# Optimization experiments

Measured on AMD Instinct MI355X. Metric: run time of the kernel, lower is better.

Reference implementation:

```python
import jax, jax.numpy as jnp
import numpy as np

EPS = 1e-5

def layernorm(x, gamma, beta):
    mu = jnp.mean(x, axis=-1, keepdims=True)
    var = jnp.var(x, axis=-1, keepdims=True)
    return (x - mu) * jax.lax.rsqrt(var + EPS) * gamma + beta

def setup_inputs() -> dict:
    key = jax.random.key(0)
    ks = jax.random.split(key, 8)
    B, N, D, H, Dh, M = 2, 2048, 768, 12, 64, 3072
    s = 0.02
    return {
        "x": jax.random.normal(ks[0], (B, N, D), jnp.float32),
        "Wqkv": jax.random.normal(ks[1], (D, 3 * H * Dh), jnp.float32) * s,
        "Wout": jax.random.normal(ks[2], (H * Dh, D), jnp.float32) * s,
        "gamma1": jnp.ones((D,), jnp.float32),
        "beta1": jnp.zeros((D,), jnp.float32),
        "gamma2": jnp.ones((D,), jnp.float32),
        "beta2": jnp.zeros((D,), jnp.float32),
        "W1": jax.random.normal(ks[3], (D, M), jnp.float32) * s,
        "b1": jnp.zeros((M,), jnp.float32),
        "W2": jax.random.normal(ks[4], (M, D), jnp.float32) * s,
        "b2": jnp.zeros((D,), jnp.float32),
        "attn_bias": jax.random.normal(ks[5], (1, H, N, N), jnp.float32) * 0.1,
    }

def reference(x, Wqkv, Wout, gamma1, beta1, gamma2, beta2, W1, b1, W2, b2, attn_bias):
    B, N, D = x.shape
    H = attn_bias.shape[1]
    Dh = Wqkv.shape[1] // (3 * H)
    scale = Dh ** -0.5
    # Attention block (pre-norm)
    h = layernorm(x, gamma1, beta1)
    qkv = h @ Wqkv                              # [B, N, 3*H*Dh]
    qkv = qkv.reshape(B, N, 3, H, Dh)
    q, k, v = (jnp.transpose(qkv[:, :, i], (0, 2, 1, 3)) for i in range(3))  # [B, H, N, Dh]
    dots = jnp.einsum('bhqd,bhkd->bhqk', q, k) * scale
    # pos_info == 'mul_att_normed'
    attn = jax.nn.softmax(dots, axis=-1) * jax.nn.softmax(attn_bias, axis=-1)
    attn = attn / jnp.sum(attn, axis=-1, keepdims=True)
    out = jnp.einsum('bhqk,bhkd->bhqd', attn, v)          # [B, H, N, Dh]
    out = jnp.transpose(out, (0, 2, 1, 3)).reshape(B, N, H * Dh)
    x = out @ Wout + x
    # FeedForward block (pre-norm)
    h = layernorm(x, gamma2, beta2)
    h = jax.nn.gelu(h @ W1 + b1, approximate=False)
    x = h @ W2 + b2 + x
    return x
```

## Files before the change

### kernel.cpp

```cpp
#include <hip/hip_runtime.h>

typedef unsigned short u16t;
typedef __bf16 bf16x8 __attribute__((ext_vector_type(8)));
typedef float  f32x4  __attribute__((ext_vector_type(4)));
typedef float  f32x16 __attribute__((ext_vector_type(16)));
typedef unsigned u32x2 __attribute__((ext_vector_type(2)));
typedef unsigned u32x4 __attribute__((ext_vector_type(4)));

#define DEV __device__ __forceinline__

DEV u16t f32_to_bf16(float f) {
    unsigned u = __float_as_uint(f);
    unsigned r = (u + 0x7FFFu + ((u >> 16) & 1u)) >> 16;
    return (u16t)r;
}
DEV float bf16_to_f32(u16t u) { return __uint_as_float((unsigned)u << 16); }

DEV unsigned cvt_pk_bf16(float lo, float hi) {
    unsigned r;
    asm("v_cvt_pk_bf16_f32 %0, %1, %2" : "=v"(r) : "v"(lo), "v"(hi));
    return r;
}

DEV float gelu_exact(float x) {
    return 0.5f * x * (1.0f + erff(x * 0.70710678118654752f));
}

DEV void glds16(const void* g, void* l) {
    __builtin_amdgcn_global_load_lds(
        (const __attribute__((address_space(1))) void*)g,
        (__attribute__((address_space(3))) void*)l, 16, 0, 0);
}

#define SCHED_FENCE() __builtin_amdgcn_sched_barrier(0)

#define WAITN_BARRIER(N)                                          \
    asm volatile("s_waitcnt vmcnt(" #N ")" ::: "memory");         \
    SCHED_FENCE();                                                \
    __builtin_amdgcn_s_barrier();                                 \
    SCHED_FENCE();

#define PLAIN_BARRIER()                                           \
    SCHED_FENCE();                                                \
    __builtin_amdgcn_s_barrier();                                 \
    SCHED_FENCE();

__global__ __launch_bounds__(256)
void ln_kernel(const float* __restrict__ x, const float* __restrict__ g,
               const float* __restrict__ b, u16t* __restrict__ out)
{
    const int row = blockIdx.x;
    const int t = threadIdx.x;
    const float* xr = x + (size_t)row * 768;
    float v0 = xr[t], v1 = xr[t + 256], v2 = xr[t + 512];
    float s = v0 + v1 + v2;
    float s2 = v0 * v0 + v1 * v1 + v2 * v2;
#pragma unroll
    for (int off = 32; off > 0; off >>= 1) {
        s  += __shfl_xor(s, off);
        s2 += __shfl_xor(s2, off);
    }
    __shared__ float sm[8];
    const int w = t >> 6;
    if ((t & 63) == 0) { sm[w] = s; sm[4 + w] = s2; }
    __syncthreads();
    s  = sm[0] + sm[1] + sm[2] + sm[3];
    s2 = sm[4] + sm[5] + sm[6] + sm[7];
    const float mu  = s * (1.0f / 768.0f);
    const float var = fmaxf(s2 * (1.0f / 768.0f) - mu * mu, 0.0f);
    const float rst = rsqrtf(var + 1e-5f);
    u16t* o = out + (size_t)row * 768;
    o[t]       = f32_to_bf16((v0 - mu) * rst * g[t]       + b[t]);
    o[t + 256] = f32_to_bf16((v1 - mu) * rst * g[t + 256] + b[t + 256]);
    o[t + 512] = f32_to_bf16((v2 - mu) * rst * g[t + 512] + b[t + 512]);
}

__global__ __launch_bounds__(256)
void transpose_all(const float* __restrict__ Wqkv, const float* __restrict__ Wout,
                   const float* __restrict__ W1, const float* __restrict__ W2,
                   u16t* __restrict__ WqkvT, u16t* __restrict__ WoutT,
                   u16t* __restrict__ W1T, u16t* __restrict__ W2T)
{
    int b = blockIdx.x;
    const float* in; u16t* out; int R, C, cx, ry;
    if (b < 432)       { in = Wqkv; out = WqkvT; R = 768;  C = 2304; cx = b % 36; ry = b / 36; }
    else if (b < 576)  { b -= 432;  in = Wout; out = WoutT; R = 768;  C = 768;  cx = b % 12; ry = b / 12; }
    else if (b < 1152) { b -= 576;  in = W1;   out = W1T;   R = 768;  C = 3072; cx = b % 48; ry = b / 48; }
    else               { b -= 1152; in = W2;   out = W2T;   R = 3072; C = 768;  cx = b % 12; ry = b / 12; }
    __shared__ float tile[64][65];
    const int c0 = cx * 64, r0 = ry * 64;
    const int t = threadIdx.x;
#pragma unroll
    for (int j = 0; j < 16; ++j) {
        const int idx = j * 256 + t;
        const int rl = idx >> 6, cl = idx & 63;
        tile[rl][cl] = in[(size_t)(r0 + rl) * C + c0 + cl];
    }
    __syncthreads();
#pragma unroll
    for (int j = 0; j < 16; ++j) {
        const int idx = j * 256 + t;
        const int cl = idx >> 6, rl = idx & 63;
        out[(size_t)(c0 + cl) * R + r0 + rl] = f32_to_bf16(tile[rl][cl]);
    }
}

template <int MODE, int TM>
__global__ __launch_bounds__(256)
void gemm_kernel(const u16t* __restrict__ A, const u16t* __restrict__ BT,
                 float* __restrict__ Cf, u16t* __restrict__ Cb,
                 const float* __restrict__ bias, const float* __restrict__ res,
                 u16t* __restrict__ Qo, u16t* __restrict__ Ko,
                 u16t* __restrict__ VTo,
                 int M, int Nn, int K)
{
    constexpr int MI = TM / 32;
    constexpr int ABYTES = TM * 64;
    constexpr int BUFB = ABYTES + 8192;
    __shared__ __align__(16) char gsm[2 * BUFB];
    const int t = threadIdx.x;
    const int w = t >> 6, lane = t & 63;
    const int l16 = lane & 15, lhi = lane >> 4;
    const int wr = w >> 1, wc = w & 1;
    const int m0 = blockIdx.x * TM, n0 = blockIdx.y * 128;

    const f32x4 fz = {0.f, 0.f, 0.f, 0.f};
    f32x4 acc[MI][4];
#pragma unroll
    for (int i = 0; i < MI; ++i)
#pragma unroll
        for (int j = 0; j < 4; ++j) acc[i][j] = fz;

    const int srow = lane >> 2;
    const int sslot = ((lane & 3) ^ ((lane >> 3) & 3)) * 16;
    const int aswz = ((lhi ^ ((l16 >> 1) & 3)) << 4);

    auto stage = [&](int bufb, int kt) {
#pragma unroll
        for (int i = 0; i < TM / 64; ++i) {
            const int row = w * (TM / 4) + i * 16 + srow;
            glds16((const char*)A + ((size_t)(m0 + row) * K + kt) * 2 + sslot,
                   gsm + bufb + w * (TM * 16) + i * 1024);
        }
#pragma unroll
        for (int i = 0; i < 2; ++i) {
            const int row = w * 32 + i * 16 + srow;
            glds16((const char*)BT + ((size_t)(n0 + row) * K + kt) * 2 + sslot,
                   gsm + bufb + ABYTES + w * 2048 + i * 1024);
        }
    };

    auto body = [&](int bufb) {
        const char* Ab = gsm + bufb;
        const char* Bb = gsm + bufb + ABYTES;
        bf16x8 af[MI], bfv[4];
#pragma unroll
        for (int i = 0; i < MI; ++i)
            af[i] = *reinterpret_cast<const bf16x8*>(
                Ab + (16 * MI * wr + 16 * i + l16) * 64 + aswz);
#pragma unroll
        for (int j = 0; j < 4; ++j)
            bfv[j] = *reinterpret_cast<const bf16x8*>(
                Bb + (64 * wc + 16 * j + l16) * 64 + aswz);
#pragma unroll
        for (int i = 0; i < MI; ++i)
#pragma unroll
            for (int j = 0; j < 4; ++j)
                acc[i][j] = __builtin_amdgcn_mfma_f32_16x16x32_bf16(
                    af[i], bfv[j], acc[i][j], 0, 0, 0);
    };

    stage(0, 0);
    int bufb = 0;
    for (int kt = 0; kt + 32 < K; kt += 32) {
        stage(bufb ^ BUFB, kt + 32);
        if constexpr (TM == 128) { WAITN_BARRIER(4) }
        else                     { WAITN_BARRIER(3) }
        body(bufb);
        PLAIN_BARRIER()
        bufb ^= BUFB;
    }
    WAITN_BARRIER(0)
    body(bufb);

    const int rb = m0 + 16 * MI * wr + 4 * lhi;
    const int cb = n0 + 64 * wc + l16;

    if constexpr (MODE == 3) {
        const int qi = n0 / 768;
        const int b = rb >> 11;
        const int nn0 = rb & 2047;
#pragma unroll
        for (int j = 0; j < 4; ++j) {
            const int c = cb - qi * 768 + 16 * j;
            const int h = c >> 6, d = c & 63;
            if (qi < 2) {
                u16t* dst = (qi == 0) ? Qo : Ko;
                const size_t base = ((size_t)(b * 12 + h) * 2048 + nn0) * 64 + d;
#pragma unroll
                for (int i = 0; i < MI; ++i)
#pragma unroll
                    for (int r = 0; r < 4; ++r)
                        dst[base + (size_t)(16 * i + r) * 64] =
                            f32_to_bf16(acc[i][j][r]);
            } else {
                u16t* dst = VTo + ((size_t)(b * 12 + h) * 64 + d) * 2048 + nn0;
#pragma unroll
                for (int i = 0; i < MI; ++i) {
                    u32x2 pr;
                    pr[0] = cvt_pk_bf16(acc[i][j][0], acc[i][j][1]);
                    pr[1] = cvt_pk_bf16(acc[i][j][2], acc[i][j][3]);
                    *reinterpret_cast<u32x2*>(dst + 16 * i) = pr;
                }
            }
        }
        return;
    }

#pragma unroll
    for (int i = 0; i < MI; ++i) {
#pragma unroll
        for (int j = 0; j < 4; ++j) {
#pragma unroll
            for (int r = 0; r < 4; ++r) {
                const int row = rb + 16 * i + r;
                const int col = cb + 16 * j;
                float v = acc[i][j][r];
                if (MODE == 0) {
                    Cf[(size_t)row * Nn + col] = v;
                } else if (MODE == 1) {
                    v += res[(size_t)row * Nn + col];
                    if (bias) v += bias[col];
                    Cf[(size_t)row * Nn + col] = v;
                } else if (MODE == 2) {
                    v = gelu_exact(v + bias[col]);
                    Cb[(size_t)row * Nn + col] = f32_to_bf16(v);
                }
            }
        }
    }
}

__global__ __launch_bounds__(256, 2)
void attn_kernel(const u16t* __restrict__ Q, const u16t* __restrict__ K,
                 const u16t* __restrict__ VT, const float* __restrict__ bias,
                 u16t* __restrict__ Opart, float* __restrict__ Lpart)
{
    const int SEQ = 2048;
    const int h = blockIdx.y;
    const int ks = blockIdx.z;
    const int t = threadIdx.x;
    const int w = t >> 6, lane = t & 63;
    const int l32 = lane & 31, hi = lane >> 5;
    const int q = blockIdx.x * 128 + w * 32 + l32;
    const int bh0 = h, bh1 = 12 + h;

    __shared__ __align__(16) char smem[65536];

    const u16t* qp0 = Q + ((size_t)bh0 * SEQ + q) * 64 + 8 * hi;
    const u16t* qp1 = Q + ((size_t)bh1 * SEQ + q) * 64 + 8 * hi;
    bf16x8 qf0[4], qf1[4];
#pragma unroll
    for (int dseg = 0; dseg < 4; ++dseg) {
        qf0[dseg] = *reinterpret_cast<const bf16x8*>(qp0 + dseg * 16);
        qf1[dseg] = *reinterpret_cast<const bf16x8*>(qp1 + dseg * 16);
    }

    const char* kg0 = (const char*)K + (size_t)bh0 * SEQ * 128;
    const char* kg1 = (const char*)K + (size_t)bh1 * SEQ * 128;
    const char* vg0 = (const char*)VT + (size_t)bh0 * 64 * 4096;
    const char* vg1 = (const char*)VT + (size_t)bh1 * 64 * 4096;
    const char* bg = (const char*)bias +
                     ((size_t)h * SEQ + blockIdx.x * 128) * 8192;

    const int srow8 = lane >> 3;
    const int sslotK = ((lane & 7) ^ srow8) * 16;
    const int vrow  = w * 16 + (lane >> 2);
    const int sslotV = ((lane & 3) ^ ((vrow >> 1) & 3)) * 16;

    auto stage_all = [&](int bb, int k0) {
#pragma unroll
        for (int i = 0; i < 4; ++i) {
            const int row = 32 * w + 8 * i + srow8;
            glds16(bg + (size_t)row * 8192 + (size_t)k0 * 4 + sslotK,
                   smem + bb + 4096 * w + i * 1024);
        }
        glds16(kg0 + (size_t)(k0 + 8 * w + srow8) * 128 + sslotK,
               smem + bb + 16384 + w * 1024);
        glds16(kg1 + (size_t)(k0 + 8 * w + srow8) * 128 + sslotK,
               smem + bb + 20480 + w * 1024);
        glds16(vg0 + (size_t)vrow * 4096 + (size_t)k0 * 2 + sslotV,
               smem + bb + 24576 + w * 1024);
        glds16(vg1 + (size_t)vrow * 4096 + (size_t)k0 * 2 + sslotV,
               smem + bb + 28672 + w * 1024);
    };

    const int rsw = l32 & 7;
    int boff[4], koff[4];
#pragma unroll
    for (int g = 0; g < 4; ++g)
        boff[g] = (32 * w + l32) * 128 + ((((g << 1) + hi) ^ rsw) << 4);
#pragma unroll
    for (int dseg = 0; dseg < 4; ++dseg)
        koff[dseg] = l32 * 128 + ((((dseg << 1) + hi) ^ rsw) << 4);
    const int vr3 = (l32 >> 1) & 3;
    const int voff00 = l32 * 64 + ((hi ^ vr3) << 4);
    const int voff01 = l32 * 64 + (((2 + hi) ^ vr3) << 4);
    const int voff10 = voff00 + 32 * 64;
    const int voff11 = voff01 + 32 * 64;

    f32x16 o00, o01, o10, o11;
#pragma unroll
    for (int i = 0; i < 16; ++i) { o00[i] = 0.f; o01[i] = 0.f;
                                   o10[i] = 0.f; o11[i] = 0.f; }
    float lsum0 = 0.f, lsum1 = 0.f;

    auto batch_body = [&](const bf16x8 (&qf)[4], int kvbase, int vbase,
                          const f32x4 (&bv)[4], f32x16& oa, f32x16& ob,
                          float& lsum) {
        f32x16 st;
#pragma unroll
        for (int i = 0; i < 16; ++i) st[i] = 0.f;
#pragma unroll
        for (int dseg = 0; dseg < 4; ++dseg) {
            bf16x8 kf = *reinterpret_cast<const bf16x8*>(
                smem + kvbase + koff[dseg]);
            st = __builtin_amdgcn_mfma_f32_32x32x16_bf16(kf, qf[dseg], st, 0, 0, 0);
        }
        unsigned pk[8];
#pragma unroll
        for (int i2 = 0; i2 < 8; ++i2) {
            const int ia = 2 * i2, ib = 2 * i2 + 1;
            const float pa = __expf(st[ia] * 0.125f + bv[ia >> 2][ia & 3]);
            const float pb = __expf(st[ib] * 0.125f + bv[ib >> 2][ib & 3]);
            lsum += pa + pb;
            pk[i2] = cvt_pk_bf16(pa, pb);
        }
        unsigned sx[8];
#pragma unroll
        for (int i2 = 0; i2 < 8; ++i2)
            sx[i2] = (unsigned)__shfl_xor((int)pk[i2], 32);
        union { unsigned u[4]; bf16x8 v; } B0, B1;
        B0.u[0] = hi ? sx[2] : pk[0];
        B0.u[1] = hi ? sx[3] : pk[1];
        B0.u[2] = hi ? pk[2] : sx[0];
        B0.u[3] = hi ? pk[3] : sx[1];
        B1.u[0] = hi ? sx[6] : pk[4];
        B1.u[1] = hi ? sx[7] : pk[5];
        B1.u[2] = hi ? pk[6] : sx[4];
        B1.u[3] = hi ? pk[7] : sx[5];
        bf16x8 v00 = *reinterpret_cast<const bf16x8*>(smem + vbase + voff00);
        bf16x8 v01 = *reinterpret_cast<const bf16x8*>(smem + vbase + voff01);
        bf16x8 v10 = *reinterpret_cast<const bf16x8*>(smem + vbase + voff10);
        bf16x8 v11 = *reinterpret_cast<const bf16x8*>(smem + vbase + voff11);
        oa = __builtin_amdgcn_mfma_f32_32x32x16_bf16(v00, B0.v, oa, 0, 0, 0);
        oa = __builtin_amdgcn_mfma_f32_32x32x16_bf16(v01, B1.v, oa, 0, 0, 0);
        ob = __builtin_amdgcn_mfma_f32_32x32x16_bf16(v10, B0.v, ob, 0, 0, 0);
        ob = __builtin_amdgcn_mfma_f32_32x32x16_bf16(v11, B1.v, ob, 0, 0, 0);
    };

    const int kbeg = ks * 512;

    stage_all(0, kbeg);
    WAITN_BARRIER(0)

    int cur = 0;
    for (int i = 0; i < 16; ++i) {
        const int k0 = kbeg + 32 * i;
        if (i < 15) {
            stage_all(cur ^ 32768, k0 + 32);
            WAITN_BARRIER(8)
        } else {
            WAITN_BARRIER(0)
        }
        {
            f32x4 bv[4];
#pragma unroll
            for (int g = 0; g < 4; ++g)
                bv[g] = *reinterpret_cast<const f32x4*>(smem + cur + boff[g]);
            batch_body(qf0, cur + 16384, cur + 24576, bv, o00, o01, lsum0);
            batch_body(qf1, cur + 20480, cur + 28672, bv, o10, o11, lsum1);
        }
        PLAIN_BARRIER()
        cur ^= 32768;
    }

    lsum0 += __shfl_xor(lsum0, 32);
    lsum1 += __shfl_xor(lsum1, 32);

#pragma unroll
    for (int beta = 0; beta < 2; ++beta) {
        const int bh = beta ? bh1 : bh0;
        const f32x16& oa = beta ? o10 : o00;
        const f32x16& ob = beta ? o11 : o01;
        const float ls = beta ? lsum1 : lsum0;
        u16t* op = Opart + ((size_t)(ks * 24 + bh) * SEQ + q) * 64;
#pragma unroll
        for (int dh = 0; dh < 2; ++dh) {
            const f32x16& o = dh ? ob : oa;
#pragma unroll
            for (int g = 0; g < 4; ++g) {
                u32x2 pr;
                pr[0] = cvt_pk_bf16(o[4 * g], o[4 * g + 1]);
                pr[1] = cvt_pk_bf16(o[4 * g + 2], o[4 * g + 3]);
                *reinterpret_cast<u32x2*>(op + dh * 32 + 8 * g + 4 * hi) = pr;
            }
        }
        if (!hi)
            Lpart[(size_t)(ks * 24 + bh) * SEQ + q] = ls;
    }
}

__global__ __launch_bounds__(256)
void attn_combine(const u16t* __restrict__ Opart,
                  const float* __restrict__ Lpart, u16t* __restrict__ out)
{
    const int idx = blockIdx.x * 256 + threadIdx.x;
    const int dg = idx & 7;
    const int q = (idx >> 3) & 2047;
    const int bh = idx >> 14;
    const int b = bh / 12, h = bh % 12;
    const size_t base = ((size_t)bh * 2048 + q) * 64 + dg * 8;
    const size_t stride = (size_t)24 * 2048 * 64;
    float acc[8] = {0.f, 0.f, 0.f, 0.f, 0.f, 0.f, 0.f, 0.f};
    float l = 0.f;
#pragma unroll
    for (int j = 0; j < 4; ++j) {
        const u32x4 a = *reinterpret_cast<const u32x4*>(Opart + base + j * stride);
#pragma unroll
        for (int m = 0; m < 4; ++m) {
            acc[2 * m]     += bf16_to_f32((u16t)(a[m] & 0xFFFF));
            acc[2 * m + 1] += bf16_to_f32((u16t)(a[m] >> 16));
        }
        l += Lpart[(size_t)j * 24 * 2048 + bh * 2048 + q];
    }
    const float inv = 1.0f / l;
    u32x4 r;
#pragma unroll
    for (int m = 0; m < 4; ++m)
        r[m] = cvt_pk_bf16(acc[2 * m] * inv, acc[2 * m + 1] * inv);
    *reinterpret_cast<u32x4*>(
        out + ((size_t)(b * 2048 + q)) * 768 + h * 64 + dg * 8) = r;
}

extern "C" void kernel_launch(void* const* d_in, const int* in_sizes, int n_in,
                              void* d_out, int out_size, void* d_ws, size_t ws_size,
                              hipStream_t stream)
{
    const float* x    = (const float*)d_in[0];
    const float* Wqkv = (const float*)d_in[1];
    const float* Wout = (const float*)d_in[2];
    const float* g1   = (const float*)d_in[3];
    const float* be1  = (const float*)d_in[4];
    const float* g2   = (const float*)d_in[5];
    const float* be2  = (const float*)d_in[6];
    const float* W1   = (const float*)d_in[7];
    const float* b1   = (const float*)d_in[8];
    const float* W2   = (const float*)d_in[9];
    const float* b2   = (const float*)d_in[10];
    const float* ab   = (const float*)d_in[11];
    float* outp = (float*)d_out;

    char* ws = (char*)d_ws;
    size_t off = 0;
    auto alloc = [&](size_t bytes) -> char* {
        char* p = ws + off;
        off += (bytes + 255) & ~(size_t)255;
        return p;
    };

    u16t* WqkvT = (u16t*)alloc((size_t)2304 * 768 * 2);
    u16t* WoutT = (u16t*)alloc((size_t)768 * 768 * 2);
    u16t* W1T   = (u16t*)alloc((size_t)3072 * 768 * 2);
    u16t* W2T   = (u16t*)alloc((size_t)768 * 3072 * 2);
    u16t* h1    = (u16t*)alloc((size_t)4096 * 768 * 2);
    u16t* Qb    = (u16t*)alloc((size_t)24 * 2048 * 64 * 2);
    u16t* Kb    = (u16t*)alloc((size_t)24 * 2048 * 64 * 2);
    u16t* VTb   = (u16t*)alloc((size_t)24 * 64 * 2048 * 2);
    u16t* attnb = (u16t*)alloc((size_t)4096 * 768 * 2);
    float* x1   = (float*)alloc((size_t)4096 * 768 * 4);
    u16t* h2    = (u16t*)alloc((size_t)4096 * 768 * 2);
    u16t* Opart = (u16t*)alloc((size_t)4 * 24 * 2048 * 64 * 2);
    float* Lpart = (float*)alloc((size_t)4 * 24 * 2048 * 4);
    u16t* act   = (u16t*)alloc((size_t)4096 * 3072 * 2);

    transpose_all<<<1728, 256, 0, stream>>>(Wqkv, Wout, W1, W2,
                                            WqkvT, WoutT, W1T, W2T);

    ln_kernel<<<4096, 256, 0, stream>>>(x, g1, be1, h1);
    gemm_kernel<3, 128><<<dim3(32, 18), 256, 0, stream>>>(
        h1, WqkvT, nullptr, nullptr, nullptr, nullptr, Qb, Kb, VTb,
        4096, 2304, 768);
    attn_kernel<<<dim3(16, 12, 4), 256, 0, stream>>>(Qb, Kb, VTb, ab, Opart, Lpart);
    attn_combine<<<(24 * 2048 * 8) / 256, 256, 0, stream>>>(Opart, Lpart, attnb);
    gemm_kernel<1, 64><<<dim3(64, 6), 256, 0, stream>>>(
        attnb, WoutT, x1, nullptr, nullptr, x, nullptr, nullptr, nullptr,
        4096, 768, 768);

    ln_kernel<<<4096, 256, 0, stream>>>(x1, g2, be2, h2);
    gemm_kernel<2, 128><<<dim3(32, 24), 256, 0, stream>>>(
        h2, W1T, nullptr, act, b1, nullptr, nullptr, nullptr, nullptr,
        4096, 3072, 768);
    gemm_kernel<1, 64><<<dim3(64, 6), 256, 0, stream>>>(
        act, W2T, outp, nullptr, b2, x1, nullptr, nullptr, nullptr,
        4096, 768, 3072);
}
```

Before: 226.5 us.

## Double GEMM K-tile to 64 with new staging layout and XOR swizzle

The GEMM main loop now stages 64-wide K slices per iteration instead of 32, doubling the A and B shared-memory buffers. Each iteration runs two MFMA sub-steps. Global-to-LDS staging is reorganised so each thread copies 16-byte chunks of 128-byte rows with an XOR swizzle over 8 slots, and the wait counts are adjusted to match. This halves the number of barriers and loop iterations per GEMM, at the cost of more LDS per block, which may reduce occupancy.

After: 226.9 us. Within noise of the previous version (+0.2%).

```diff
diff --git a/kernel.cpp b/kernel.cpp
--- a/kernel.cpp
+++ b/kernel.cpp
@@ -115,8 +115,8 @@
                  int M, int Nn, int K)
 {
     constexpr int MI = TM / 32;
-    constexpr int ABYTES = TM * 64;
-    constexpr int BUFB = ABYTES + 8192;
+    constexpr int ABYTES = TM * 128;
+    constexpr int BUFB = ABYTES + 16384;
     __shared__ __align__(16) char gsm[2 * BUFB];
     const int t = threadIdx.x;
     const int w = t >> 6, lane = t & 63;
@@ -131,51 +131,58 @@
 #pragma unroll
         for (int j = 0; j < 4; ++j) acc[i][j] = fz;
 
-    const int srow = lane >> 2;
-    const int sslot = ((lane & 3) ^ ((lane >> 3) & 3)) * 16;
-    const int aswz = ((lhi ^ ((l16 >> 1) & 3)) << 4);
+    const int rbase = t >> 3;
+    const int ssrc = ((t & 7) ^ (rbase & 7)) * 16;
 
     auto stage = [&](int bufb, int kt) {
 #pragma unroll
-        for (int i = 0; i < TM / 64; ++i) {
-            const int row = w * (TM / 4) + i * 16 + srow;
-            glds16((const char*)A + ((size_t)(m0 + row) * K + kt) * 2 + sslot,
-                   gsm + bufb + w * (TM * 16) + i * 1024);
-        }
-#pragma unroll
-        for (int i = 0; i < 2; ++i) {
-            const int row = w * 32 + i * 16 + srow;
-            glds16((const char*)BT + ((size_t)(n0 + row) * K + kt) * 2 + sslot,
-                   gsm + bufb + ABYTES + w * 2048 + i * 1024);
+        for (int i = 0; i < TM / 32; ++i) {
+            const int row = i * 32 + rbase;
+            glds16((const char*)A + ((size_t)(m0 + row) * K + kt) * 2 + ssrc,
+                   gsm + bufb + i * 4096 + t * 16);
+        }
+#pragma unroll
+        for (int i = 0; i < 4; ++i) {
+            const int row = i * 32 + rbase;
+            glds16((const char*)BT + ((size_t)(n0 + row) * K + kt) * 2 + ssrc,
+                   gsm + bufb + ABYTES + i * 4096 + t * 16);
         }
     };
 
     auto body = [&](int bufb) {
         const char* Ab = gsm + bufb;
         const char* Bb = gsm + bufb + ABYTES;
-        bf16x8 af[MI], bfv[4];
-#pragma unroll
-        for (int i = 0; i < MI; ++i)
-            af[i] = *reinterpret_cast<const bf16x8*>(
-                Ab + (16 * MI * wr + 16 * i + l16) * 64 + aswz);
-#pragma unroll
-        for (int j = 0; j < 4; ++j)
-            bfv[j] = *reinterpret_cast<const bf16x8*>(
-                Bb + (64 * wc + 16 * j + l16) * 64 + aswz);
-#pragma unroll
-        for (int i = 0; i < MI; ++i)
-#pragma unroll
-            for (int j = 0; j < 4; ++j)
-                acc[i][j] = __builtin_amdgcn_mfma_f32_16x16x32_bf16(
-                    af[i], bfv[j], acc[i][j], 0, 0, 0);
+#pragma unroll
+        for (int ks = 0; ks < 2; ++ks) {
+            const int wsl = lhi + 4 * ks;
+            bf16x8 af[MI], bfv[4];
+#pragma unroll
+            for (int i = 0; i < MI; ++i) {
+                const int row = 16 * MI * wr + 16 * i + l16;
+                af[i] = *reinterpret_cast<const bf16x8*>(
+                    Ab + row * 128 + ((wsl ^ (row & 7)) << 4));
+            }
+#pragma unroll
+            for (int j = 0; j < 4; ++j) {
+                const int row = 64 * wc + 16 * j + l16;
+                bfv[j] = *reinterpret_cast<const bf16x8*>(
+                    Bb + row * 128 + ((wsl ^ (row & 7)) << 4));
+            }
+#pragma unroll
+            for (int i = 0; i < MI; ++i)
+#pragma unroll
+                for (int j = 0; j < 4; ++j)
+                    acc[i][j] = __builtin_amdgcn_mfma_f32_16x16x32_bf16(
+                        af[i], bfv[j], acc[i][j], 0, 0, 0);
+        }
     };
 
     stage(0, 0);
     int bufb = 0;
-    for (int kt = 0; kt + 32 < K; kt += 32) {
-        stage(bufb ^ BUFB, kt + 32);
-        if constexpr (TM == 128) { WAITN_BARRIER(4) }
-        else                     { WAITN_BARRIER(3) }
+    for (int kt = 0; kt + 64 < K; kt += 64) {
+        stage(bufb ^ BUFB, kt + 64);
+        if constexpr (TM == 128) { WAITN_BARRIER(8) }
+        else                     { WAITN_BARRIER(6) }
         body(bufb);
         PLAIN_BARRIER()
         bufb ^= BUFB;
```
